# Kernel tuning notes

Measured on AMD Instinct MI355X. Metric: run time of the kernel, lower is better.

Reference implementation:

```python
import jax, jax.numpy as jnp
import numpy as np

NUM_NODES = 4096
EMBED_DIM = 64
IN_DIM = 256
OUT_DIM = 256
BATCH = 32


def setup_inputs() -> dict:
    key = jax.random.key(0)
    k1, k2, k3 = jax.random.split(key, 3)
    x = jax.random.normal(k1, (BATCH, NUM_NODES, IN_DIM), dtype=jnp.float32)
    node_ids = jnp.arange(NUM_NODES, dtype=jnp.int64)
    emb_table = jax.random.normal(k2, (NUM_NODES, EMBED_DIM), dtype=jnp.float32) * 0.1
    W = jax.random.normal(k3, (IN_DIM, OUT_DIM), dtype=jnp.float32) * (1.0 / np.sqrt(IN_DIM))
    b = jnp.zeros((OUT_DIM,), dtype=jnp.float32)
    return {"x": x, "node_ids": node_ids, "emb_table": emb_table, "W": W, "b": b}


def reference(x, node_ids, emb_table, W, b):
    # Embedding lookup for node ids -> [N, E]
    E = emb_table[node_ids]
    # Adaptive adjacency from embeddings: softmax(relu(E E^T)) over neighbors
    logits = jax.nn.relu(jnp.einsum("ne,me->nm", E, E))  # [N, N]
    adj = jax.nn.softmax(logits, axis=-1)
    # Graph convolution: aggregate neighbor features, then linear + relu
    h = jnp.einsum("nm,bmd->bnd", adj, x)          # [B, N, in_dim]
    out = jax.nn.relu(jnp.einsum("bnd,do->bno", h, W) + b)  # [B, N, out_dim]
    return out
```

## Files before the change

kernel.cpp:

```cpp
#include <hip/hip_runtime.h>

#define NN   4096
#define ED   64
#define DIN  256
#define DOUT 256
#define NB   32

typedef __attribute__((ext_vector_type(8))) short bf16x8;
typedef __attribute__((ext_vector_type(4))) float f32x4;

__device__ __forceinline__ unsigned short f2bf(float f) {
    union { float f; unsigned u; } v; v.f = f;
    unsigned r = v.u + 0x7FFF + ((v.u >> 16) & 1);
    return (unsigned short)(r >> 16);
}
__device__ __forceinline__ float bf2f(unsigned short s) {
    union { unsigned u; float f; } v; v.u = ((unsigned)s) << 16;
    return v.f;
}

#define GLDS16(g, l) __builtin_amdgcn_global_load_lds( \
    (const __attribute__((address_space(1))) void*)(g), \
    (__attribute__((address_space(3))) void*)(l), 16, 0, 0)

__device__ __forceinline__ void fma4(float4& d, float s, const float4& v) {
    d.x = fmaf(s, v.x, d.x);
    d.y = fmaf(s, v.y, d.y);
    d.z = fmaf(s, v.z, d.z);
    d.w = fmaf(s, v.w, d.w);
}

__global__ void k_gather(const float* __restrict__ emb, const int* __restrict__ ids,
                         float* __restrict__ E) {
    int n = blockIdx.x;
    int e = threadIdx.x;
    int id = ids[n];
    id = id < 0 ? 0 : (id >= NN ? NN - 1 : id);
    E[(size_t)n * ED + e] = emb[(size_t)id * ED + e];
}

__global__ __launch_bounds__(256) void k_logits(const float* __restrict__ E,
                                                unsigned short* __restrict__ adjbf) {
    __shared__ __align__(16) float Ea[ED][64 + 4];
    __shared__ __align__(16) float Eb[ED][64 + 4];
    const int tid = threadIdx.x;
    const int ty = tid >> 4, tx = tid & 15;
    const int rb = blockIdx.x, cb = blockIdx.y;

    #pragma unroll
    for (int k = 0; k < 4; ++k) {
        int l = tid + k * 256;
        int row = l >> 4;
        int kq = (l & 15) * 4;
        float4 va = *(const float4*)&E[(size_t)(rb * 64 + row) * ED + kq];
        Ea[kq + 0][row] = va.x; Ea[kq + 1][row] = va.y;
        Ea[kq + 2][row] = va.z; Ea[kq + 3][row] = va.w;
        float4 vb = *(const float4*)&E[(size_t)(cb * 64 + row) * ED + kq];
        Eb[kq + 0][row] = vb.x; Eb[kq + 1][row] = vb.y;
        Eb[kq + 2][row] = vb.z; Eb[kq + 3][row] = vb.w;
    }
    __syncthreads();

    float4 acc[4] = {};
    #pragma unroll
    for (int k = 0; k < ED; ++k) {
        float4 ar = *(const float4*)&Ea[k][ty * 4];
        float4 br = *(const float4*)&Eb[k][tx * 4];
        fma4(acc[0], ar.x, br);
        fma4(acc[1], ar.y, br);
        fma4(acc[2], ar.z, br);
        fma4(acc[3], ar.w, br);
    }

    #pragma unroll
    for (int i = 0; i < 4; ++i) {
        float4 v = acc[i];
        ushort4 s;
        s.x = f2bf(fmaxf(v.x, 0.f)); s.y = f2bf(fmaxf(v.y, 0.f));
        s.z = f2bf(fmaxf(v.z, 0.f)); s.w = f2bf(fmaxf(v.w, 0.f));
        size_t n = (size_t)(rb * 64 + ty * 4 + i);
        *(ushort4*)&adjbf[n * NN + cb * 64 + tx * 4] = s;
    }
}

__global__ __launch_bounds__(256) void k_softmax(unsigned short* __restrict__ adj) {
    __shared__ float red[256];
    const int tid = threadIdx.x;
    const size_t base = (size_t)blockIdx.x * NN + (size_t)tid * 16;

    unsigned short t16[16];
    *(uint4*)&t16[0] = *(const uint4*)&adj[base];
    *(uint4*)&t16[8] = *(const uint4*)&adj[base + 8];
    float v[16];
    float mx = 0.0f;
    #pragma unroll
    for (int j = 0; j < 16; ++j) { v[j] = bf2f(t16[j]); mx = fmaxf(mx, v[j]); }

    red[tid] = mx; __syncthreads();
    for (int off = 128; off > 0; off >>= 1) {
        if (tid < off) red[tid] = fmaxf(red[tid], red[tid + off]);
        __syncthreads();
    }
    mx = red[0];
    __syncthreads();

    float s = 0.f;
    #pragma unroll
    for (int j = 0; j < 16; ++j) { v[j] = expf(v[j] - mx); s += v[j]; }
    red[tid] = s; __syncthreads();
    for (int off = 128; off > 0; off >>= 1) {
        if (tid < off) red[tid] += red[tid + off];
        __syncthreads();
    }
    const float inv = 1.0f / red[0];

    #pragma unroll
    for (int j = 0; j < 16; ++j) t16[j] = f2bf(v[j] * inv);
    *(uint4*)&adj[base]     = *(const uint4*)&t16[0];
    *(uint4*)&adj[base + 8] = *(const uint4*)&t16[8];
}

__global__ void k_wt(const float* __restrict__ W, unsigned short* __restrict__ WT) {
    int m = blockIdx.x;
    int k = threadIdx.x;
    WT[(size_t)m * DIN + k] = f2bf(W[(size_t)k * DOUT + m]);
}

__global__ __launch_bounds__(256) void k_y(const unsigned short* __restrict__ WT,
                                           const float* __restrict__ x,
                                           unsigned short* __restrict__ yT) {
    __shared__ __align__(16) short As[128 * 32];
    __shared__ __align__(16) short Bs[128 * 32];
    const int tid = threadIdx.x;
    const int lane = tid & 63, w = tid >> 6;
    const int wr = (w >> 1) * 64, wc = (w & 1) * 64;
    const int fr = lane & 15, fq = lane >> 4;
    const int m0 = blockIdx.x * 128;
    const int n0 = blockIdx.y * 128;
    const int b  = blockIdx.z;
    const float* xb = x + (size_t)b * NN * DIN;
    const int brow = tid >> 1, bh = (tid & 1) * 16;

    f32x4 acc[4][4];
    #pragma unroll
    for (int i = 0; i < 4; ++i)
        #pragma unroll
        for (int j = 0; j < 4; ++j) acc[i][j] = (f32x4){0.f, 0.f, 0.f, 0.f};

    for (int k0 = 0; k0 < DIN; k0 += 32) {
        __syncthreads();
        #pragma unroll
        for (int i = 0; i < 2; ++i) {
            int idx = (w * 2 + i) * 512 + lane * 8;
            int row = idx >> 5, kk = idx & 31;
            GLDS16(WT + (size_t)(m0 + row) * DIN + k0 + kk, &As[(w * 2 + i) * 512]);
        }
        float fv[16];
        *(float4*)&fv[0]  = *(const float4*)&xb[(size_t)(n0 + brow) * DIN + k0 + bh + 0];
        *(float4*)&fv[4]  = *(const float4*)&xb[(size_t)(n0 + brow) * DIN + k0 + bh + 4];
        *(float4*)&fv[8]  = *(const float4*)&xb[(size_t)(n0 + brow) * DIN + k0 + bh + 8];
        *(float4*)&fv[12] = *(const float4*)&xb[(size_t)(n0 + brow) * DIN + k0 + bh + 12];
        unsigned u[8];
        #pragma unroll
        for (int j = 0; j < 8; ++j)
            u[j] = (unsigned)f2bf(fv[2 * j]) | ((unsigned)f2bf(fv[2 * j + 1]) << 16);
        *(uint4*)&Bs[brow * 32 + bh]     = make_uint4(u[0], u[1], u[2], u[3]);
        *(uint4*)&Bs[brow * 32 + bh + 8] = make_uint4(u[4], u[5], u[6], u[7]);
        __syncthreads();

        bf16x8 a[4], bb[4];
        #pragma unroll
        for (int mi = 0; mi < 4; ++mi)
            a[mi] = *(const bf16x8*)&As[(wr + mi * 16 + fr) * 32 + fq * 8];
        #pragma unroll
        for (int ni = 0; ni < 4; ++ni)
            bb[ni] = *(const bf16x8*)&Bs[(wc + ni * 16 + fr) * 32 + fq * 8];
        #pragma unroll
        for (int mi = 0; mi < 4; ++mi)
            #pragma unroll
            for (int ni = 0; ni < 4; ++ni)
                acc[mi][ni] = __builtin_amdgcn_mfma_f32_16x16x32_bf16(
                    a[mi], bb[ni], acc[mi][ni], 0, 0, 0);
    }

    unsigned short* yb = yT + (size_t)b * DOUT * NN;
    #pragma unroll
    for (int mi = 0; mi < 4; ++mi)
        #pragma unroll
        for (int ni = 0; ni < 4; ++ni)
            #pragma unroll
            for (int r = 0; r < 4; ++r) {
                int row = m0 + wr + mi * 16 + fq * 4 + r;
                int col = n0 + wc + ni * 16 + fr;
                yb[(size_t)row * NN + col] = f2bf(acc[mi][ni][r]);
            }
}

__global__ __launch_bounds__(512, 2) void k_gcn(const unsigned short* __restrict__ adj,
                                                const unsigned short* __restrict__ yT,
                                                const float* __restrict__ bias,
                                                float* __restrict__ out) {
    __shared__ __align__(16) char smem[131072];

    const int tid  = threadIdx.x;
    const int lane = tid & 63, wid = tid >> 6;
    const int fr = lane & 15, fq = lane >> 4;
    const int wr = wid >> 2, wc = wid & 3;
    const int m0 = blockIdx.x * 256;
    const int by = blockIdx.y;

    const char* Apanel = (const char*)(adj + (size_t)m0 * NN);
    const char* Bpanel = (const char*)(yT + (size_t)by * DOUT * NN);

    #define STAGE4(gpan, ktb, ldsb)                                              \
        {                                                                        \
            _Pragma("unroll")                                                    \
            for (int c = 0; c < 4; ++c) {                                        \
                int bo  = c * 8192 + wid * 1024 + lane * 16;                     \
                int row = bo >> 7;                                               \
                int scol = (bo & 127) ^ ((row & 7) << 4);                        \
                GLDS16((gpan) + (size_t)row * 8192 + (ktb) + scol,               \
                       (ldsb) + c * 8192 + wid * 1024);                          \
            }                                                                    \
        }

    STAGE4(Bpanel, 0,   smem + 32768);
    STAGE4(Apanel, 0,   smem);
    STAGE4(Bpanel, 128, smem + 65536 + 32768);
    STAGE4(Apanel, 128, smem + 65536);

    f32x4 acc[8][4];
    #pragma unroll
    for (int i = 0; i < 8; ++i)
        #pragma unroll
        for (int j = 0; j < 4; ++j) acc[i][j] = (f32x4){0.f, 0.f, 0.f, 0.f};

    const int xorp0 = (fq << 4) ^ ((fr & 7) << 4);
    const int xorp1 = (64 | (fq << 4)) ^ ((fr & 7) << 4);
    const int abase = (wr * 128 + fr) * 128;
    const int bbase = (wc * 64 + fr) * 128;

    for (int j = 0; j < 64; ++j) {
        char* bufA = smem + (j & 1) * 65536;
        char* bufB = bufA + 32768;

        if (j + 1 < 64) { asm volatile("s_waitcnt vmcnt(8)" ::: "memory"); }
        else            { asm volatile("s_waitcnt vmcnt(0)" ::: "memory"); }
        asm volatile("s_barrier" ::: "memory");

        bf16x8 Br[4][2], A0[4][2], A1[4][2];
        #pragma unroll
        for (int ni = 0; ni < 4; ++ni) {
            Br[ni][0] = *(const bf16x8*)(bufB + bbase + ni * 2048 + xorp0);
            Br[ni][1] = *(const bf16x8*)(bufB + bbase + ni * 2048 + xorp1);
        }
        #pragma unroll
        for (int mi = 0; mi < 4; ++mi) {
            A0[mi][0] = *(const bf16x8*)(bufA + abase + mi * 2048 + xorp0);
            A0[mi][1] = *(const bf16x8*)(bufA + abase + mi * 2048 + xorp1);
        }
        #pragma unroll
        for (int mi = 0; mi < 4; ++mi) {
            A1[mi][0] = *(const bf16x8*)(bufA + abase + 8192 + mi * 2048 + xorp0);
            A1[mi][1] = *(const bf16x8*)(bufA + abase + 8192 + mi * 2048 + xorp1);
        }

        __builtin_amdgcn_s_setprio(1);
        #pragma unroll
        for (int mi = 0; mi < 4; ++mi)
            #pragma unroll
            for (int ni = 0; ni < 4; ++ni) {
                acc[mi][ni] = __builtin_amdgcn_mfma_f32_16x16x32_bf16(A0[mi][0], Br[ni][0], acc[mi][ni], 0, 0, 0);
                acc[mi][ni] = __builtin_amdgcn_mfma_f32_16x16x32_bf16(A0[mi][1], Br[ni][1], acc[mi][ni], 0, 0, 0);
            }
        #pragma unroll
        for (int mi = 0; mi < 4; ++mi)
            #pragma unroll
            for (int ni = 0; ni < 4; ++ni) {
                acc[4 + mi][ni] = __builtin_amdgcn_mfma_f32_16x16x32_bf16(A1[mi][0], Br[ni][0], acc[4 + mi][ni], 0, 0, 0);
                acc[4 + mi][ni] = __builtin_amdgcn_mfma_f32_16x16x32_bf16(A1[mi][1], Br[ni][1], acc[4 + mi][ni], 0, 0, 0);
            }
        __builtin_amdgcn_s_setprio(0);

        asm volatile("s_waitcnt lgkmcnt(0)" ::: "memory");
        asm volatile("s_barrier" ::: "memory");
        if (j + 2 < 64) {
            STAGE4(Bpanel, (j + 2) * 128, bufB);
            STAGE4(Apanel, (j + 2) * 128, bufA);
        }
    }

    float bv[4];
    #pragma unroll
    for (int ni = 0; ni < 4; ++ni) bv[ni] = bias[wc * 64 + ni * 16 + fr];

    #pragma unroll
    for (int am = 0; am < 8; ++am) {
        const int node = m0 + wr * 128 + am * 16 + fq * 4;
        #pragma unroll
        for (int ni = 0; ni < 4; ++ni) {
            const int dcol = wc * 64 + ni * 16 + fr;
            #pragma unroll
            for (int rr = 0; rr < 4; ++rr) {
                float vv = acc[am][ni][rr] + bv[ni];
                out[((size_t)by * NN + node + rr) * DOUT + dcol] = fmaxf(vv, 0.f);
            }
        }
    }
    #undef STAGE4
}

extern "C" void kernel_launch(void* const* d_in, const int* in_sizes, int n_in,
                              void* d_out, int out_size, void* d_ws, size_t ws_size,
                              hipStream_t stream) {
    const float* x    = (const float*)d_in[0];
    const int*   ids  = (const int*)d_in[1];
    const float* emb  = (const float*)d_in[2];
    const float* W    = (const float*)d_in[3];
    const float* bias = (const float*)d_in[4];
    float* out = (float*)d_out;

    char* ws = (char*)d_ws;
    unsigned short* adjbf = (unsigned short*)ws;
    float*          E     = (float*)(ws + 33554432);
    unsigned short* WT    = (unsigned short*)(ws + 33554432 + 1048576);
    unsigned short* yT    = (unsigned short*)(ws + 33554432 + 1048576 + 131072);

    k_gather  <<<NN, ED, 0, stream>>>(emb, ids, E);
    k_logits  <<<dim3(NN / 64, NN / 64), 256, 0, stream>>>(E, adjbf);
    k_softmax <<<NN, 256, 0, stream>>>(adjbf);
    k_wt      <<<DOUT, DIN, 0, stream>>>(W, WT);
    k_y       <<<dim3(DOUT / 128, NN / 128, NB), 256, 0, stream>>>(WT, x, yT);
    k_gcn     <<<dim3(16, 32), 512, 0, stream>>>(adjbf, yT, bias, out);
}
```

Before: 350.9 us.

## Interleave LDS fragment loads with MFMA quarters across a software-pipelined K loop

Restructures the main GEMM K-loop into a software pipeline. The loop is unrolled by two over the double buffer, and the MFMA work is split into quarters that run while the next A/B fragments are read from LDS, with sched_barriers enforcing the order. The last quarter of each tile is deferred into the next tile so LDS reads and global prefetch overlap with matrix-core work. The cost is more live registers (extra B fragment sets) and more complex waitcnt and barrier ordering.

```diff
diff --git a/kernel.cpp b/kernel.cpp
--- a/kernel.cpp
+++ b/kernel.cpp
@@ -240,55 +240,79 @@
     const int abase = (wr * 128 + fr) * 128;
     const int bbase = (wc * 64 + fr) * 128;
 
-    for (int j = 0; j < 64; ++j) {
-        char* bufA = smem + (j & 1) * 65536;
-        char* bufB = bufA + 32768;
-
-        if (j + 1 < 64) { asm volatile("s_waitcnt vmcnt(8)" ::: "memory"); }
-        else            { asm volatile("s_waitcnt vmcnt(0)" ::: "memory"); }
-        asm volatile("s_barrier" ::: "memory");
-
-        bf16x8 Br[4][2], A0[4][2], A1[4][2];
-        #pragma unroll
-        for (int ni = 0; ni < 4; ++ni) {
-            Br[ni][0] = *(const bf16x8*)(bufB + bbase + ni * 2048 + xorp0);
-            Br[ni][1] = *(const bf16x8*)(bufB + bbase + ni * 2048 + xorp1);
-        }
-        #pragma unroll
-        for (int mi = 0; mi < 4; ++mi) {
-            A0[mi][0] = *(const bf16x8*)(bufA + abase + mi * 2048 + xorp0);
-            A0[mi][1] = *(const bf16x8*)(bufA + abase + mi * 2048 + xorp1);
-        }
-        #pragma unroll
-        for (int mi = 0; mi < 4; ++mi) {
-            A1[mi][0] = *(const bf16x8*)(bufA + abase + 8192 + mi * 2048 + xorp0);
-            A1[mi][1] = *(const bf16x8*)(bufA + abase + 8192 + mi * 2048 + xorp1);
-        }
-
-        __builtin_amdgcn_s_setprio(1);
-        #pragma unroll
-        for (int mi = 0; mi < 4; ++mi)
-            #pragma unroll
-            for (int ni = 0; ni < 4; ++ni) {
-                acc[mi][ni] = __builtin_amdgcn_mfma_f32_16x16x32_bf16(A0[mi][0], Br[ni][0], acc[mi][ni], 0, 0, 0);
-                acc[mi][ni] = __builtin_amdgcn_mfma_f32_16x16x32_bf16(A0[mi][1], Br[ni][1], acc[mi][ni], 0, 0, 0);
-            }
-        #pragma unroll
-        for (int mi = 0; mi < 4; ++mi)
-            #pragma unroll
-            for (int ni = 0; ni < 4; ++ni) {
-                acc[4 + mi][ni] = __builtin_amdgcn_mfma_f32_16x16x32_bf16(A1[mi][0], Br[ni][0], acc[4 + mi][ni], 0, 0, 0);
-                acc[4 + mi][ni] = __builtin_amdgcn_mfma_f32_16x16x32_bf16(A1[mi][1], Br[ni][1], acc[4 + mi][ni], 0, 0, 0);
-            }
-        __builtin_amdgcn_s_setprio(0);
-
-        asm volatile("s_waitcnt lgkmcnt(0)" ::: "memory");
-        asm volatile("s_barrier" ::: "memory");
-        if (j + 2 < 64) {
-            STAGE4(Bpanel, (j + 2) * 128, bufB);
-            STAGE4(Apanel, (j + 2) * 128, bufA);
-        }
-    }
+    bf16x8 A0[4][2], A1[4][2], B01[2][2], B23[2][2][2];
+
+#define MFMA_Q(AOFF, ASET, NOFF, BSET)                                           \
+    __builtin_amdgcn_s_setprio(1);                                               \
+    _Pragma("unroll")                                                            \
+    for (int mi = 0; mi < 4; ++mi)                                               \
+        _Pragma("unroll")                                                        \
+        for (int ni = 0; ni < 2; ++ni) {                                         \
+            acc[(AOFF) + mi][(NOFF) + ni] = __builtin_amdgcn_mfma_f32_16x16x32_bf16( \
+                ASET[mi][0], BSET[ni][0], acc[(AOFF) + mi][(NOFF) + ni], 0, 0, 0);   \
+            acc[(AOFF) + mi][(NOFF) + ni] = __builtin_amdgcn_mfma_f32_16x16x32_bf16( \
+                ASET[mi][1], BSET[ni][1], acc[(AOFF) + mi][(NOFF) + ni], 0, 0, 0);   \
+        }                                                                        \
+    __builtin_amdgcn_s_setprio(0);
+
+#define TILE(PAR)                                                                \
+    {                                                                            \
+        char* bufA = smem + (PAR) * 65536;                                       \
+        char* bufB = bufA + 32768;                                               \
+        const int j = jt * 2 + (PAR);                                            \
+        if ((PAR) == 0 || jt < 31) { asm volatile("s_waitcnt vmcnt(8)" ::: "memory"); } \
+        else                       { asm volatile("s_waitcnt vmcnt(0)" ::: "memory"); } \
+        asm volatile("s_barrier" ::: "memory");                                  \
+                         \
+        _Pragma("unroll")                                                        \
+        for (int mi = 0; mi < 4; ++mi) {                                         \
+            A0[mi][0] = *(const bf16x8*)(bufA + abase + mi * 2048 + xorp0);      \
+            A0[mi][1] = *(const bf16x8*)(bufA + abase + mi * 2048 + xorp1);      \
+        }                                                                        \
+        _Pragma("unroll")                                                        \
+        for (int ni = 0; ni < 2; ++ni) {                                         \
+            B01[ni][0] = *(const bf16x8*)(bufB + bbase + ni * 2048 + xorp0);     \
+            B01[ni][1] = *(const bf16x8*)(bufB + bbase + ni * 2048 + xorp1);     \
+        }                                                                        \
+        __builtin_amdgcn_sched_barrier(0);                                       \
+        if ((PAR) == 1 || jt > 0) { MFMA_Q(4, A1, 2, (B23[1 - (PAR)])) }         \
+                                          \
+        asm volatile("s_waitcnt lgkmcnt(0)" ::: "memory");                       \
+        __builtin_amdgcn_sched_barrier(0);                                       \
+        _Pragma("unroll")                                                        \
+        for (int ni = 0; ni < 2; ++ni) {                                         \
+            B23[(PAR)][ni][0] = *(const bf16x8*)(bufB + bbase + (2 + ni) * 2048 + xorp0); \
+            B23[(PAR)][ni][1] = *(const bf16x8*)(bufB + bbase + (2 + ni) * 2048 + xorp1); \
+        }                                                                        \
+        __builtin_amdgcn_sched_barrier(0);                                       \
+        MFMA_Q(0, A0, 0, B01)                                                    \
+                                              \
+        asm volatile("s_waitcnt lgkmcnt(0)" ::: "memory");                       \
+        __builtin_amdgcn_sched_barrier(0);                                       \
+        _Pragma("unroll")                                                        \
+        for (int mi = 0; mi < 4; ++mi) {                                         \
+            A1[mi][0] = *(const bf16x8*)(bufA + abase + 8192 + mi * 2048 + xorp0); \
+            A1[mi][1] = *(const bf16x8*)(bufA + abase + 8192 + mi * 2048 + xorp1); \
+        }                                                                        \
+        __builtin_amdgcn_sched_barrier(0);                                       \
+        MFMA_Q(0, A0, 2, (B23[(PAR)]))                                           \
+                                     \
+        asm volatile("s_waitcnt lgkmcnt(0)" ::: "memory");                       \
+        __builtin_amdgcn_sched_barrier(0);                                       \
+        asm volatile("s_barrier" ::: "memory");                                  \
+        if (jt < 31) {                                                           \
+            STAGE4(Bpanel, (j + 2) * 128, bufB);                                 \
+            STAGE4(Apanel, (j + 2) * 128, bufA);                                 \
+        }                                                                        \
+        __builtin_amdgcn_sched_barrier(0);                                       \
+        MFMA_Q(4, A1, 0, B01)                                                    \
+    }
+
+    for (int jt = 0; jt < 32; ++jt) {
+        TILE(0)
+        TILE(1)
+    }
+    MFMA_Q(4, A1, 2, (B23[1]))
 
     float bv[4];
     #pragma unroll
@@ -308,6 +332,8 @@
         }
     }
     #undef STAGE4
+    #undef TILE
+    #undef MFMA_Q
 }
 
 extern "C" void kernel_launch(void* const* d_in, const int* in_sizes, int n_in,
```

Result: slower. 550.0 us (+56.7%).

## Split K-tile into half-stages and interleave LDS reads, global loads, and MFMA

Applied to the files above, without the earlier changes.

Restructures the main GEMM loop so each 128-element K tile is handled as two 64-wide halves, each in its own LDS sub-buffer with a new XOR swizzle. Global-to-LDS loads for the next halves are issued between LDS fragment reads and MFMA groups, with sched_barriers and extra s_barriers. The aim is to overlap memory traffic with tensor-core work at a finer grain and cut the register footprint of fragments. In exchange it adds more block-wide barriers per iteration and more complex vmcnt bookkeeping that could stall or race.

```diff
diff --git a/kernel.cpp b/kernel.cpp
--- a/kernel.cpp
+++ b/kernel.cpp
@@ -212,82 +212,97 @@
     const char* Apanel = (const char*)(adj + (size_t)m0 * NN);
     const char* Bpanel = (const char*)(yT + (size_t)by * DOUT * NN);
 
-    #define STAGE4(gpan, ktb, ldsb)                                              \
-        {                                                                        \
+    #define STAGE_HALF(gpan, ktb, KS, ldsb)                                      \
+        { _Pragma("unroll")                                                      \
+          for (int h = 0; h < 2; ++h) {                                          \
+              int r = h * 128 + wid * 16 + (lane >> 2);                          \
+              int gcol = (((lane & 3) ^ ((r >> 1) & 3)) << 4);                   \
+              GLDS16((gpan) + (size_t)r * 8192 + (ktb) + (KS) * 64 + gcol,       \
+                     (ldsb) + (KS) * 16384 + h * 8192 + wid * 1024);             \
+          } }
+
+    STAGE_HALF(Apanel, 0,   0, smem);
+    STAGE_HALF(Bpanel, 0,   0, smem + 32768);
+    STAGE_HALF(Apanel, 0,   1, smem);
+    STAGE_HALF(Bpanel, 0,   1, smem + 32768);
+    STAGE_HALF(Apanel, 128, 0, smem + 65536);
+    STAGE_HALF(Bpanel, 128, 0, smem + 65536 + 32768);
+
+    f32x4 acc[8][4];
+    #pragma unroll
+    for (int i = 0; i < 8; ++i)
+        #pragma unroll
+        for (int j = 0; j < 4; ++j) acc[i][j] = (f32x4){0.f, 0.f, 0.f, 0.f};
+
+    const int chunksw = ((fq ^ ((fr >> 1) & 3)) << 4);
+    const int arow = (wr * 128 + fr) * 64 + chunksw;
+    const int brow = (wc * 64  + fr) * 64 + chunksw;
+
+    #define READ_A(dst, RB0, KS)                                                 \
+        _Pragma("unroll")                                                        \
+        for (int mi = 0; mi < 4; ++mi)                                           \
+            dst[mi] = *(const bf16x8*)(bufA + (KS) * 16384 + arow + ((RB0) + mi) * 1024);
+    #define READ_B(dst, KS)                                                      \
+        _Pragma("unroll")                                                        \
+        for (int ni = 0; ni < 4; ++ni)                                           \
+            dst[ni] = *(const bf16x8*)(bufB + (KS) * 16384 + brow + ni * 1024);
+    #define MFMA16(AOFF, Aset, Bset)                                             \
+        __builtin_amdgcn_s_setprio(1);                                           \
+        _Pragma("unroll")                                                        \
+        for (int mi = 0; mi < 4; ++mi)                                           \
             _Pragma("unroll")                                                    \
-            for (int c = 0; c < 4; ++c) {                                        \
-                int bo  = c * 8192 + wid * 1024 + lane * 16;                     \
-                int row = bo >> 7;                                               \
-                int scol = (bo & 127) ^ ((row & 7) << 4);                        \
-                GLDS16((gpan) + (size_t)row * 8192 + (ktb) + scol,               \
-                       (ldsb) + c * 8192 + wid * 1024);                          \
-            }                                                                    \
-        }
-
-    STAGE4(Bpanel, 0,   smem + 32768);
-    STAGE4(Apanel, 0,   smem);
-    STAGE4(Bpanel, 128, smem + 65536 + 32768);
-    STAGE4(Apanel, 128, smem + 65536);
-
-    f32x4 acc[8][4];
-    #pragma unroll
-    for (int i = 0; i < 8; ++i)
-        #pragma unroll
-        for (int j = 0; j < 4; ++j) acc[i][j] = (f32x4){0.f, 0.f, 0.f, 0.f};
-
-    const int xorp0 = (fq << 4) ^ ((fr & 7) << 4);
-    const int xorp1 = (64 | (fq << 4)) ^ ((fr & 7) << 4);
-    const int abase = (wr * 128 + fr) * 128;
-    const int bbase = (wc * 64 + fr) * 128;
-
-    for (int j = 0; j < 64; ++j) {
-        char* bufA = smem + (j & 1) * 65536;
-        char* bufB = bufA + 32768;
-
-        if (j + 1 < 64) { asm volatile("s_waitcnt vmcnt(8)" ::: "memory"); }
-        else            { asm volatile("s_waitcnt vmcnt(0)" ::: "memory"); }
-        asm volatile("s_barrier" ::: "memory");
-
-        bf16x8 Br[4][2], A0[4][2], A1[4][2];
-        #pragma unroll
-        for (int ni = 0; ni < 4; ++ni) {
-            Br[ni][0] = *(const bf16x8*)(bufB + bbase + ni * 2048 + xorp0);
-            Br[ni][1] = *(const bf16x8*)(bufB + bbase + ni * 2048 + xorp1);
-        }
-        #pragma unroll
-        for (int mi = 0; mi < 4; ++mi) {
-            A0[mi][0] = *(const bf16x8*)(bufA + abase + mi * 2048 + xorp0);
-            A0[mi][1] = *(const bf16x8*)(bufA + abase + mi * 2048 + xorp1);
-        }
-        #pragma unroll
-        for (int mi = 0; mi < 4; ++mi) {
-            A1[mi][0] = *(const bf16x8*)(bufA + abase + 8192 + mi * 2048 + xorp0);
-            A1[mi][1] = *(const bf16x8*)(bufA + abase + 8192 + mi * 2048 + xorp1);
-        }
-
-        __builtin_amdgcn_s_setprio(1);
-        #pragma unroll
-        for (int mi = 0; mi < 4; ++mi)
-            #pragma unroll
-            for (int ni = 0; ni < 4; ++ni) {
-                acc[mi][ni] = __builtin_amdgcn_mfma_f32_16x16x32_bf16(A0[mi][0], Br[ni][0], acc[mi][ni], 0, 0, 0);
-                acc[mi][ni] = __builtin_amdgcn_mfma_f32_16x16x32_bf16(A0[mi][1], Br[ni][1], acc[mi][ni], 0, 0, 0);
-            }
-        #pragma unroll
-        for (int mi = 0; mi < 4; ++mi)
-            #pragma unroll
-            for (int ni = 0; ni < 4; ++ni) {
-                acc[4 + mi][ni] = __builtin_amdgcn_mfma_f32_16x16x32_bf16(A1[mi][0], Br[ni][0], acc[4 + mi][ni], 0, 0, 0);
-                acc[4 + mi][ni] = __builtin_amdgcn_mfma_f32_16x16x32_bf16(A1[mi][1], Br[ni][1], acc[4 + mi][ni], 0, 0, 0);
-            }
+            for (int ni = 0; ni < 4; ++ni)                                       \
+                acc[(AOFF) + mi][ni] = __builtin_amdgcn_mfma_f32_16x16x32_bf16(  \
+                    Aset[mi], Bset[ni], acc[(AOFF) + mi][ni], 0, 0, 0);          \
         __builtin_amdgcn_s_setprio(0);
 
+    asm volatile("s_waitcnt vmcnt(8)" ::: "memory");
+    asm volatile("s_barrier" ::: "memory");
+
+    for (int t = 0; t < 64; ++t) {
+        char* bufA  = smem + (t & 1) * 65536;
+        char* bufB  = bufA + 32768;
+        char* nbufA = smem + ((t + 1) & 1) * 65536;
+        char* nbufB = nbufA + 32768;
+        bf16x8 Af[4], Bf[4];
+
+        READ_B(Bf, 0);
+        READ_A(Af, 0, 0);
+        if (t + 1 < 64) STAGE_HALF(Apanel, (t + 1) * 128, 1, nbufA);
+        asm volatile("s_barrier" ::: "memory");
         asm volatile("s_waitcnt lgkmcnt(0)" ::: "memory");
-        asm volatile("s_barrier" ::: "memory");
-        if (j + 2 < 64) {
-            STAGE4(Bpanel, (j + 2) * 128, bufB);
-            STAGE4(Apanel, (j + 2) * 128, bufA);
-        }
+        __builtin_amdgcn_sched_barrier(0);
+        MFMA16(0, Af, Bf);
+        asm volatile("s_barrier" ::: "memory");
+
+        READ_A(Af, 4, 0);
+        if (t + 1 < 64) STAGE_HALF(Bpanel, (t + 1) * 128, 1, nbufB);
+        asm volatile("s_barrier" ::: "memory");
+        asm volatile("s_waitcnt lgkmcnt(0)" ::: "memory");
+        __builtin_amdgcn_sched_barrier(0);
+        MFMA16(4, Af, Bf);
+        if (t < 63) { asm volatile("s_waitcnt vmcnt(8)" ::: "memory"); }
+        else        { asm volatile("s_waitcnt vmcnt(0)" ::: "memory"); }
+        asm volatile("s_barrier" ::: "memory");
+
+        READ_B(Bf, 1);
+        READ_A(Af, 0, 1);
+        if (t + 2 < 64) STAGE_HALF(Apanel, (t + 2) * 128, 0, bufA);
+        asm volatile("s_barrier" ::: "memory");
+        asm volatile("s_waitcnt lgkmcnt(0)" ::: "memory");
+        __builtin_amdgcn_sched_barrier(0);
+        MFMA16(0, Af, Bf);
+        asm volatile("s_barrier" ::: "memory");
+
+        READ_A(Af, 4, 1);
+        if (t + 2 < 64) STAGE_HALF(Bpanel, (t + 2) * 128, 0, bufB);
+        asm volatile("s_barrier" ::: "memory");
+        asm volatile("s_waitcnt lgkmcnt(0)" ::: "memory");
+        __builtin_amdgcn_sched_barrier(0);
+        MFMA16(4, Af, Bf);
+        if (t < 62)       { asm volatile("s_waitcnt vmcnt(8)" ::: "memory"); }
+        else if (t == 62) { asm volatile("s_waitcnt vmcnt(4)" ::: "memory"); }
+        asm volatile("s_barrier" ::: "memory");
     }
 
     float bv[4];
@@ -307,7 +322,10 @@
             }
         }
     }
-    #undef STAGE4
+    #undef STAGE_HALF
+    #undef READ_A
+    #undef READ_B
+    #undef MFMA16
 }
 
 extern "C" void kernel_launch(void* const* d_in, const int* in_sizes, int n_in,
```

After: 344.4 us. Within noise of the previous version (-1.9%).
